# Performance work log

Hardware: AMD Instinct MI355X
Metric: run time of the kernel (lower is better)

The kernel has to match this reference:

```python
import jax, jax.numpy as jnp
import numpy as np

GAMMA = 0.999   # from TDLoss.__init__ default
LAMBDA = 0.95   # from compute_gae default lambda_
B, S = 8192, 2048


def setup_inputs() -> dict:
    key = jax.random.key(0)
    k1, k2, k3, k4 = jax.random.split(key, 4)
    rewards = jax.random.normal(k1, (B, S), dtype=jnp.float32)
    values = jax.random.normal(k2, (B, S), dtype=jnp.float32)
    dones = jax.random.randint(k3, (B, S), 0, 2).astype(jnp.int32)
    # prefix validity mask: valid_len[b] = mask[b].sum(), as assumed by compute_gae
    lengths = jax.random.randint(k4, (B,), S // 2, S + 1)
    mask = (jnp.arange(S)[None, :] < lengths[:, None]).astype(jnp.int32)
    return {"rewards": rewards, "values": values, "dones": dones, "mask": mask}


def _gae(rewards, values, dones_f, mask, gamma, lam):
    # rewards/values/dones_f: [B,S] float; mask: [B,S] int prefix mask
    b, s = rewards.shape
    valid_len = mask.sum(axis=1)                      # [B]
    t_idx = jnp.arange(s)
    valid = t_idx[None, :] < valid_len[:, None]       # [B,S] bool
    is_last = t_idx[None, :] == (valid_len[:, None] - 1)
    # next_value = values[:, t+1], except 0 at the last valid step (and at t=S-1)
    next_vals = jnp.concatenate([values[:, 1:], jnp.zeros((b, 1), values.dtype)], axis=1)
    next_vals = jnp.where(is_last, jnp.zeros((), values.dtype), next_vals)
    nd = 1.0 - dones_f                                # (1 - done)
    delta = rewards + gamma * next_vals * nd - values

    def step(gae, xs):
        d_t, nd_t, valid_t = xs                        # each [B]
        g = d_t + gamma * lam * nd_t * gae
        g = jnp.where(valid_t, g, jnp.zeros((), d_t.dtype))  # zero outside valid prefix; resets carry
        return g, g

    xs = (delta.T, nd.T, valid.T)                     # time-major [S,B]
    _, adv_t = jax.lax.scan(step, jnp.zeros(b, rewards.dtype), xs, reverse=True)
    advantages = adv_t.T                              # [B,S]
    returns = jnp.where(valid, advantages + values, jnp.zeros((), values.dtype))
    return advantages, returns


def reference(rewards, values, dones, mask):
    return _gae(rewards, values, dones.astype(jnp.float32), mask, GAMMA, LAMBDA)
```

## Files before the change

### kernel.cpp

```cpp
#include <hip/hip_runtime.h>


static constexpr int BATCH = 8192;
static constexpr int SEQ   = 2048;
static constexpr int TBLK  = 256;
static constexpr int NBLK  = SEQ / TBLK;
static constexpr float GAMMA  = 0.999f;
static constexpr float LAMBDA = 0.95f;
static constexpr float GL     = GAMMA * LAMBDA;

__global__ __launch_bounds__(256, 4) void gae_kernel(
    const float* __restrict__ rewards,
    const float* __restrict__ values,
    const int*   __restrict__ dones,
    const int*   __restrict__ mask,
    float*       __restrict__ out)
{
    const int lane = threadIdx.x & 63;
    const int row  = blockIdx.x * 4 + (threadIdx.x >> 6);
    const size_t rowbase = (size_t)row * SEQ;

    float C    = 0.0f;
    float edge = 0.0f;

    for (int j = NBLK - 1; j >= 0; --j) {
        const size_t off = rowbase + (size_t)j * TBLK + (size_t)lane * 4;

        const float4 r4 = *reinterpret_cast<const float4*>(rewards + off);
        const float4 v4 = *reinterpret_cast<const float4*>(values  + off);
        const int4   d4 = *reinterpret_cast<const int4*>(dones + off);
        const int4   m4 = *reinterpret_cast<const int4*>(mask  + off);

        const float rr[4] = {r4.x, r4.y, r4.z, r4.w};
        const float vv[4] = {v4.x, v4.y, v4.z, v4.w};
        const int   dd[4] = {d4.x, d4.y, d4.z, d4.w};
        const int   mm[4] = {m4.x, m4.y, m4.z, m4.w};

        float a[4], b[4], vm[4];
        float mr[4], mnd[4];
        #pragma unroll
        for (int e = 0; e < 4; ++e) {
            const bool m  = (mm[e] != 0);
            const bool mn = m && (dd[e] == 0);
            vm[e]  = m ? vv[e] : 0.0f;
            mr[e]  = m ? rr[e] : 0.0f;
            mnd[e] = mn ? 1.0f : 0.0f;
            a[e]   = mn ? GL : 0.0f;
        }
        float nv3 = __shfl_down(vm[0], 1, 64);
        if (lane == 63) nv3 = edge;
        const float nv[4] = {vm[1], vm[2], vm[3], nv3};
        #pragma unroll
        for (int e = 0; e < 4; ++e)
            b[e] = mr[e] + GAMMA * nv[e] * mnd[e] - vm[e];

        float A = a[3], B = b[3];
        #pragma unroll
        for (int e = 2; e >= 0; --e) {
            B = fmaf(a[e], B, b[e]);
            A = a[e] * A;
        }

        float As = A, Bs = B;
        #pragma unroll
        for (int d = 1; d < 64; d <<= 1) {
            const float Ao = __shfl_down(As, d, 64);
            const float Bo = __shfl_down(Bs, d, 64);
            if (lane + d < 64) {
                Bs = fmaf(As, Bo, Bs);
                As = As * Ao;
            }
        }
        const float A0 = __shfl(As, 0, 64);
        const float B0 = __shfl(Bs, 0, 64);
        float cA = __shfl_down(As, 1, 64);
        float cB = __shfl_down(Bs, 1, 64);
        if (lane == 63) { cA = 1.0f; cB = 0.0f; }
        float g = fmaf(cA, C, cB);

        float adv[4], ret[4];
        #pragma unroll
        for (int e = 3; e >= 0; --e) {
            g = fmaf(a[e], g, b[e]);
            adv[e] = g;
            ret[e] = g + vm[e];
        }

        C    = fmaf(A0, C, B0);
        edge = __shfl(vm[0], 0, 64);

        *reinterpret_cast<float4*>(out + off) =
            make_float4(adv[0], adv[1], adv[2], adv[3]);
        *reinterpret_cast<float4*>(out + (size_t)BATCH * SEQ + off) =
            make_float4(ret[0], ret[1], ret[2], ret[3]);
    }
}

extern "C" void kernel_launch(void* const* d_in, const int* in_sizes, int n_in,
                              void* d_out, int out_size, void* d_ws, size_t ws_size,
                              hipStream_t stream) {
    const float* rewards = (const float*)d_in[0];
    const float* values  = (const float*)d_in[1];
    const int*   dones   = (const int*)d_in[2];
    const int*   mask    = (const int*)d_in[3];
    float* out = (float*)d_out;

    dim3 grid(BATCH / 4), block(256);
    gae_kernel<<<grid, block, 0, stream>>>(rewards, values, dones, mask, out);
}
```

Baseline: 319.9 us.

## Scan each row with one block of four wavefronts instead of a sequential chunk loop

Each row is now handled by a whole 256-thread block. Every wavefront covers a 512-element segment, with 8 elements per lane. Segment carries and boundary values are combined through shared memory and two barriers, replacing the serial eight-chunk loop per wavefront. This raises parallelism and memory-level concurrency, since all loads issue at once, and removes the loop-carried dependency. The cost is four times as many blocks plus block-wide synchronisation. The delta term is also refactored to use a*(1/lambda), which gives gamma*(1-done)*mask through an FMA.

```diff
diff --git a/kernel.cpp b/kernel.cpp
--- a/kernel.cpp
+++ b/kernel.cpp
@@ -3,11 +3,10 @@
 
 static constexpr int BATCH = 8192;
 static constexpr int SEQ   = 2048;
-static constexpr int TBLK  = 256;
-static constexpr int NBLK  = SEQ / TBLK;
-static constexpr float GAMMA  = 0.999f;
-static constexpr float LAMBDA = 0.95f;
-static constexpr float GL     = GAMMA * LAMBDA;
+static constexpr float GAMMA      = 0.999f;
+static constexpr float LAMBDA     = 0.95f;
+static constexpr float GL         = GAMMA * LAMBDA;
+static constexpr float INV_LAMBDA = 1.0f / LAMBDA;
 
 __global__ __launch_bounds__(256, 4) void gae_kernel(
     const float* __restrict__ rewards,
@@ -16,84 +15,99 @@
     const int*   __restrict__ mask,
     float*       __restrict__ out)
 {
-    const int lane = threadIdx.x & 63;
-    const int row  = blockIdx.x * 4 + (threadIdx.x >> 6);
-    const size_t rowbase = (size_t)row * SEQ;
+    const int tid  = threadIdx.x;
+    const int lane = tid & 63;
+    const int w    = tid >> 6;
+    const size_t rowbase = (size_t)blockIdx.x * SEQ;
+    const size_t off = rowbase + (size_t)w * 512 + (size_t)lane * 8;
 
-    float C    = 0.0f;
-    float edge = 0.0f;
+    __shared__ float s_edge[4];
+    __shared__ float s_Aw[4];
+    __shared__ float s_Bw[4];
 
-    for (int j = NBLK - 1; j >= 0; --j) {
-        const size_t off = rowbase + (size_t)j * TBLK + (size_t)lane * 4;
+    const float4 r0 = *reinterpret_cast<const float4*>(rewards + off);
+    const float4 r1 = *reinterpret_cast<const float4*>(rewards + off + 4);
+    const float4 v0 = *reinterpret_cast<const float4*>(values  + off);
+    const float4 v1 = *reinterpret_cast<const float4*>(values  + off + 4);
+    const int4   d0 = *reinterpret_cast<const int4*>(dones + off);
+    const int4   d1 = *reinterpret_cast<const int4*>(dones + off + 4);
+    const int4   m0 = *reinterpret_cast<const int4*>(mask  + off);
+    const int4   m1 = *reinterpret_cast<const int4*>(mask  + off + 4);
 
-        const float4 r4 = *reinterpret_cast<const float4*>(rewards + off);
-        const float4 v4 = *reinterpret_cast<const float4*>(values  + off);
-        const int4   d4 = *reinterpret_cast<const int4*>(dones + off);
-        const int4   m4 = *reinterpret_cast<const int4*>(mask  + off);
+    const float rr[8] = {r0.x, r0.y, r0.z, r0.w, r1.x, r1.y, r1.z, r1.w};
+    const float vv[8] = {v0.x, v0.y, v0.z, v0.w, v1.x, v1.y, v1.z, v1.w};
+    const int   dd[8] = {d0.x, d0.y, d0.z, d0.w, d1.x, d1.y, d1.z, d1.w};
+    const int   mm[8] = {m0.x, m0.y, m0.z, m0.w, m1.x, m1.y, m1.z, m1.w};
 
-        const float rr[4] = {r4.x, r4.y, r4.z, r4.w};
-        const float vv[4] = {v4.x, v4.y, v4.z, v4.w};
-        const int   dd[4] = {d4.x, d4.y, d4.z, d4.w};
-        const int   mm[4] = {m4.x, m4.y, m4.z, m4.w};
+    float a[8], b[8], vm[8];
+    #pragma unroll
+    for (int e = 0; e < 8; ++e) {
+        const bool m  = (mm[e] != 0);
+        const bool mn = m && (dd[e] == 0);
+        vm[e] = m ? vv[e] : 0.0f;
+        a[e]  = mn ? GL : 0.0f;
+        b[e]  = (m ? rr[e] : 0.0f) - vm[e];
+    }
 
-        float a[4], b[4], vm[4];
-        float mr[4], mnd[4];
-        #pragma unroll
-        for (int e = 0; e < 4; ++e) {
-            const bool m  = (mm[e] != 0);
-            const bool mn = m && (dd[e] == 0);
-            vm[e]  = m ? vv[e] : 0.0f;
-            mr[e]  = m ? rr[e] : 0.0f;
-            mnd[e] = mn ? 1.0f : 0.0f;
-            a[e]   = mn ? GL : 0.0f;
+    if (lane == 0) s_edge[w] = vm[0];
+    __syncthreads();
+
+    float nv7 = __shfl_down(vm[0], 1, 64);
+    if (lane == 63) nv7 = (w < 3) ? s_edge[w + 1] : 0.0f;
+
+    #pragma unroll
+    for (int e = 0; e < 8; ++e) {
+        const float nv = (e < 7) ? vm[e + 1] : nv7;
+        b[e] = fmaf(a[e] * INV_LAMBDA, nv, b[e]);
+    }
+
+    float A = a[7], B = b[7];
+    #pragma unroll
+    for (int e = 6; e >= 0; --e) {
+        B = fmaf(a[e], B, b[e]);
+        A *= a[e];
+    }
+
+    float As = A, Bs = B;
+    #pragma unroll
+    for (int d = 1; d < 64; d <<= 1) {
+        const float Ao = __shfl_down(As, d, 64);
+        const float Bo = __shfl_down(Bs, d, 64);
+        if (lane + d < 64) {
+            Bs = fmaf(As, Bo, Bs);
+            As *= Ao;
         }
-        float nv3 = __shfl_down(vm[0], 1, 64);
-        if (lane == 63) nv3 = edge;
-        const float nv[4] = {vm[1], vm[2], vm[3], nv3};
-        #pragma unroll
-        for (int e = 0; e < 4; ++e)
-            b[e] = mr[e] + GAMMA * nv[e] * mnd[e] - vm[e];
+    }
 
-        float A = a[3], B = b[3];
-        #pragma unroll
-        for (int e = 2; e >= 0; --e) {
-            B = fmaf(a[e], B, b[e]);
-            A = a[e] * A;
-        }
+    if (lane == 0) { s_Aw[w] = As; s_Bw[w] = Bs; }
+    __syncthreads();
 
-        float As = A, Bs = B;
-        #pragma unroll
-        for (int d = 1; d < 64; d <<= 1) {
-            const float Ao = __shfl_down(As, d, 64);
-            const float Bo = __shfl_down(Bs, d, 64);
-            if (lane + d < 64) {
-                Bs = fmaf(As, Bo, Bs);
-                As = As * Ao;
-            }
-        }
-        const float A0 = __shfl(As, 0, 64);
-        const float B0 = __shfl(Bs, 0, 64);
-        float cA = __shfl_down(As, 1, 64);
-        float cB = __shfl_down(Bs, 1, 64);
-        if (lane == 63) { cA = 1.0f; cB = 0.0f; }
-        float g = fmaf(cA, C, cB);
+    float C = 0.0f;
+    for (int u = 3; u > w; --u)
+        C = fmaf(s_Aw[u], C, s_Bw[u]);
 
-        float adv[4], ret[4];
-        #pragma unroll
-        for (int e = 3; e >= 0; --e) {
-            g = fmaf(a[e], g, b[e]);
-            adv[e] = g;
-            ret[e] = g + vm[e];
-        }
+    float cA = __shfl_down(As, 1, 64);
+    float cB = __shfl_down(Bs, 1, 64);
+    if (lane == 63) { cA = 1.0f; cB = 0.0f; }
+    float g = fmaf(cA, C, cB);
 
-        C    = fmaf(A0, C, B0);
-        edge = __shfl(vm[0], 0, 64);
+    float adv[8], ret[8];
+    #pragma unroll
+    for (int e = 7; e >= 0; --e) {
+        g = fmaf(a[e], g, b[e]);
+        adv[e] = g;
+        ret[e] = g + vm[e];
+    }
 
-        *reinterpret_cast<float4*>(out + off) =
-            make_float4(adv[0], adv[1], adv[2], adv[3]);
-        *reinterpret_cast<float4*>(out + (size_t)BATCH * SEQ + off) =
-            make_float4(ret[0], ret[1], ret[2], ret[3]);
-    }
+    *reinterpret_cast<float4*>(out + off) =
+        make_float4(adv[0], adv[1], adv[2], adv[3]);
+    *reinterpret_cast<float4*>(out + off + 4) =
+        make_float4(adv[4], adv[5], adv[6], adv[7]);
+    const size_t roff = (size_t)BATCH * SEQ + off;
+    *reinterpret_cast<float4*>(out + roff) =
+        make_float4(ret[0], ret[1], ret[2], ret[3]);
+    *reinterpret_cast<float4*>(out + roff + 4) =
+        make_float4(ret[4], ret[5], ret[6], ret[7]);
 }
 
 extern "C" void kernel_launch(void* const* d_in, const int* in_sizes, int n_in,
@@ -105,6 +119,6 @@
     const int*   mask    = (const int*)d_in[3];
     float* out = (float*)d_out;
 
-    dim3 grid(BATCH / 4), block(256);
+    dim3 grid(BATCH), block(256);
     gae_kernel<<<grid, block, 0, stream>>>(rewards, values, dones, mask, out);
 }
```

New measurement: 321.5 us. About the same (+0.5%).
